# Performance work log

Hardware: AMD Instinct MI355X
Metric: run time of the kernel (lower is better)

## Reference

```python
import jax, jax.numpy as jnp
import numpy as np
import math

N_NODES = 50000
N_EDGES = 600000
EMBED_DIM = 128


def setup_inputs() -> dict:
    key = jax.random.key(0)
    k_emb, k_edge, k_w = jax.random.split(key, 3)
    emb = jax.random.normal(k_emb, (N_NODES, EMBED_DIM), dtype=jnp.float32) * 0.1
    edges = jax.random.randint(k_edge, (2, N_EDGES), 0, N_NODES, dtype=jnp.int64)
    std = 1.0 / math.sqrt(EMBED_DIM)
    # nn.Linear(2*embed_dim, embed_dim): weight [out, in]
    W = jax.random.uniform(k_w, (EMBED_DIM, 2 * EMBED_DIM), dtype=jnp.float32,
                           minval=-std, maxval=std)
    b = jnp.zeros((EMBED_DIM,), dtype=jnp.float32)
    gamma = jnp.ones((EMBED_DIM,), dtype=jnp.float32)
    beta = jnp.zeros((EMBED_DIM,), dtype=jnp.float32)
    return {"emb": emb, "edges": edges, "W": W, "b": b, "gamma": gamma, "beta": beta}


def reference(emb, edges, W, b, gamma, beta):
    bsz = emb.shape[0]
    row = edges[0]  # destination / output node per edge (spmm row index)
    col = edges[1]  # source node per edge (spmm col index)
    # edge attention logits: <emb[dst], emb[src]> per edge, then exp
    attn = jnp.exp(jnp.sum(emb[row] * emb[col], axis=-1))  # [E]
    # special_spmm with ones -> per-row sum of attention weights
    denom = jax.ops.segment_sum(attn, row, num_segments=bsz)  # [N]
    # special_spmm with emb -> exp-weighted scatter-add of source embeddings
    agg = jax.ops.segment_sum(attn[:, None] * emb[col], row, num_segments=bsz)  # [N, D]
    agg = agg / (denom[:, None] + 1e-20)
    # concat + linear
    x = jnp.concatenate([emb, agg], axis=-1) @ W.T + b  # [N, D]
    # layer norm (eps=1e-5, affine)
    mu = jnp.mean(x, axis=-1, keepdims=True)
    var = jnp.mean((x - mu) ** 2, axis=-1, keepdims=True)
    x = (x - mu) * jax.lax.rsqrt(var + 1e-5) * gamma + beta
    return x
```

## Files before the change

kernel.cpp:

```cpp
#include <hip/hip_runtime.h>
#include <math.h>

#define D 128
#define TWO_D 256
#define CAP 64
#define CCAP 3584
#define CHUNK 2048

typedef __bf16 v8bf __attribute__((ext_vector_type(8)));
typedef float  v4f  __attribute__((ext_vector_type(4)));
typedef unsigned short us4 __attribute__((ext_vector_type(4)));
typedef unsigned short v8us __attribute__((ext_vector_type(8)));

#define OFF_CNT      0u
#define OFF_COLBUF   200192u
#define OFF_CCNT     6600192u
#define OFF_COARSE   6601216u
#define OFF_WBF16    10271232u
#define OFF_EMBB     10336768u
#define WS_TIER_A    23136768u

__global__ __launch_bounds__(256) void k_cvt_bin(
    const float* __restrict__ emb, const float* __restrict__ W,
    const int* __restrict__ edges,
    __bf16* __restrict__ embb, __bf16* __restrict__ Wb,
    unsigned int* __restrict__ ccnt, unsigned int* __restrict__ coarse,
    int nEmb8, int nW8, int E, int binB, int NB)
{
    if ((int)blockIdx.x < binB) {
        __shared__ unsigned int hist[256];
        __shared__ unsigned int base[256];
        int tid = threadIdx.x;
        int e0  = blockIdx.x * CHUNK;
        hist[tid] = 0;
        __syncthreads();

        unsigned rs[CHUNK / 256];
        #pragma unroll
        for (int k = 0; k < CHUNK / 256; ++k) {
            int e = e0 + k * 256 + tid;
            if (e < E) {
                unsigned r  = (unsigned)edges[e];
                unsigned lp = atomicAdd(&hist[r >> 8], 1u);
                rs[k] = (r << 12) | lp;
            }
        }
        __syncthreads();
        if (tid < NB) {
            unsigned h = hist[tid];
            base[tid] = h ? atomicAdd(&ccnt[tid], h) : 0u;
        }
        __syncthreads();
        #pragma unroll
        for (int k = 0; k < CHUNK / 256; ++k) {
            int e = e0 + k * 256 + tid;
            if (e < E) {
                unsigned pk = rs[k];
                unsigned r  = pk >> 12;
                unsigned lp = pk & 0xFFFu;
                unsigned c  = (unsigned)edges[E + e];
                int bk = r >> 8;
                unsigned slot = base[bk] + lp;
                if (slot < CCAP)
                    coarse[(size_t)bk * CCAP + slot] = ((r & 255u) << 16) | c;
            }
        }
    } else {
        int tid = ((int)blockIdx.x - binB) * 256 + threadIdx.x;
        if (tid < nEmb8 + nW8) {
            const float* src;
            __bf16* dst;
            if (tid < nEmb8) { src = emb + (size_t)tid * 8; dst = embb + (size_t)tid * 8; }
            else { int j = (tid - nEmb8) * 8; src = W + j; dst = Wb + j; }
            float4 f0 = *(const float4*)(src);
            float4 f1 = *(const float4*)(src + 4);
            v8bf v;
            v[0] = (__bf16)f0.x; v[1] = (__bf16)f0.y; v[2] = (__bf16)f0.z; v[3] = (__bf16)f0.w;
            v[4] = (__bf16)f1.x; v[5] = (__bf16)f1.y; v[6] = (__bf16)f1.z; v[7] = (__bf16)f1.w;
            *(v8bf*)dst = v;
        }
    }
}

__global__ __launch_bounds__(256) void k_fine(
    const unsigned int* __restrict__ coarse,
    const unsigned int* __restrict__ ccnt,
    int* __restrict__ cnt, unsigned short* __restrict__ colbuf, int N)
{
    __shared__ __align__(16) unsigned short ftile[256 * CAP];
    __shared__ unsigned int fcnt[256];
    int tid = threadIdx.x;
    int b   = blockIdx.x;
    int r0  = b << 8;
    fcnt[tid] = 0;
    __syncthreads();

    unsigned mc = ccnt[b];
    if (mc > CCAP) mc = CCAP;
    for (unsigned i = tid; i < mc; i += 256) {
        unsigned p = coarse[(size_t)b * CCAP + i];
        unsigned rlo = p >> 16;
        unsigned c   = p & 0xFFFFu;
        unsigned lp  = atomicAdd(&fcnt[rlo], 1u);
        if (lp < CAP) ftile[rlo * CAP + lp] = (unsigned short)c;
    }
    __syncthreads();

    int r = r0 + tid;
    if (r < N) {
        unsigned d = fcnt[tid];
        cnt[r] = (int)(d > CAP ? CAP : d);
    }
    #pragma unroll
    for (int j = 0; j < 8; ++j) {
        int g  = j * 256 + tid;
        int rr = r0 + (g >> 3);
        if (rr < N)
            *(v8us*)(colbuf + (size_t)rr * CAP + (g & 7) * 8) =
                *(const v8us*)(ftile + (g >> 3) * CAP + (g & 7) * 8);
    }
}

__global__ __launch_bounds__(256) void gcn_agg_b(
    const __bf16* __restrict__ embb,
    const unsigned short* __restrict__ colbuf,
    const int* __restrict__ cnt,
    __bf16* __restrict__ aggb,
    int N)
{
    int wid  = threadIdx.x >> 6;
    int lane = threadIdx.x & 63;
    int il   = lane & 15;
    int slot = lane >> 4;
    int n    = blockIdx.x * 4 + wid;
    if (n >= N) return;

    v8bf a8 = *(const v8bf*)(embb + (size_t)n * D + il * 8);
    float af[8];
    #pragma unroll
    for (int q = 0; q < 8; ++q) af[q] = (float)a8[q];

    float acc[8];
    #pragma unroll
    for (int q = 0; q < 8; ++q) acc[q] = 0.f;
    float den = 0.f;

    int deg = cnt[n];
    if (deg > CAP) deg = CAP;
    const unsigned short* row = colbuf + (size_t)n * CAP;
    int nb = (deg + 7) >> 3;

    int i0 = 0, i1 = 0;
    if (slot < deg)     i0 = (int)row[slot];
    if (slot + 4 < deg) i1 = (int)row[slot + 4];
    v8bf r0 = *(const v8bf*)(embb + (size_t)i0 * D + il * 8);
    v8bf r1 = *(const v8bf*)(embb + (size_t)i1 * D + il * 8);

    for (int b = 0; b < nb; ++b) {
        int e   = b * 8;
        int rem = deg - e;
        bool v0 = (slot < rem);
        bool v1 = (slot + 4 < rem);

        int en   = e + 8;
        int remn = deg - en;
        bool hn  = (b + 1 < nb);
        int j0 = (hn && slot < remn)     ? (int)row[en + slot]     : 0;
        int j1 = (hn && slot + 4 < remn) ? (int)row[en + slot + 4] : 0;
        v8bf p0 = *(const v8bf*)(embb + (size_t)j0 * D + il * 8);
        v8bf p1 = *(const v8bf*)(embb + (size_t)j1 * D + il * 8);

        float f0[8], f1[8];
        #pragma unroll
        for (int q = 0; q < 8; ++q) { f0[q] = (float)r0[q]; f1[q] = (float)r1[q]; }
        float t0 = 0.f, t1 = 0.f;
        #pragma unroll
        for (int q = 0; q < 8; ++q) { t0 += af[q] * f0[q]; t1 += af[q] * f1[q]; }
        #pragma unroll
        for (int off = 1; off <= 8; off <<= 1) {
            t0 += __shfl_xor(t0, off, 16);
            t1 += __shfl_xor(t1, off, 16);
        }
        float w0 = v0 ? __expf(t0) : 0.f;
        float w1 = v1 ? __expf(t1) : 0.f;
        #pragma unroll
        for (int q = 0; q < 8; ++q) acc[q] += w0 * f0[q] + w1 * f1[q];
        den += w0 + w1;

        r0 = p0; r1 = p1;
    }

    #pragma unroll
    for (int q = 0; q < 8; ++q) {
        acc[q] += __shfl_xor(acc[q], 16, 64);
        acc[q] += __shfl_xor(acc[q], 32, 64);
    }
    den += __shfl_xor(den, 16, 64);
    den += __shfl_xor(den, 32, 64);

    if (slot == 0) {
        float inv = 1.0f / (den + 1e-20f);
        v8bf r;
        #pragma unroll
        for (int q = 0; q < 8; ++q) r[q] = (__bf16)(acc[q] * inv);
        *(v8bf*)(aggb + (size_t)n * 256 + il * 8) = r;
    }
}

__global__ __launch_bounds__(256) void gcn_node_b(
    const __bf16* __restrict__ embb,
    const __bf16* __restrict__ Wb,
    const float* __restrict__ bias,
    const float* __restrict__ gamma,
    const float* __restrict__ beta,
    float* __restrict__ out, int N)
{
    __shared__ __align__(16) __bf16 xt[64 * 256];

    int t    = threadIdx.x;
    int wave = t >> 6;
    int lane = t & 63;
    int n0   = blockIdx.x * 64;
    const __bf16* aggb = (const __bf16*)out;

    #pragma unroll
    for (int j = 0; j < 8; ++j) {
        int gf = j * 64 + lane;
        int ml = gf >> 5;
        int m  = wave * 16 + ml;
        int g  = gf & 31;
        int n  = n0 + m;
        v8bf v;
        if (n < N) {
            v = (g < 16) ? *(const v8bf*)(embb + (size_t)n * D + g * 8)
                         : *(const v8bf*)(aggb + (size_t)n * 256 + (g - 16) * 8);
        } else {
            #pragma unroll
            for (int q = 0; q < 8; ++q) v[q] = (__bf16)0.0f;
        }
        *(v8bf*)(xt + (m * 32 + (g ^ (m & 7))) * 8) = v;
    }

    int mrow = lane & 15;
    int quad = lane >> 4;
    int mloc = wave * 16 + mrow;

    v8bf a[8];
    #pragma unroll
    for (int kt = 0; kt < 8; ++kt) {
        int g = (kt * 4 + quad) ^ (mloc & 7);
        a[kt] = *(const v8bf*)(xt + (mloc * 32 + g) * 8);
    }

    float bi[8], gm[8], bt[8];
    #pragma unroll
    for (int ft = 0; ft < 8; ++ft) {
        int f = ft * 16 + mrow;
        bi[ft] = bias[f]; gm[ft] = gamma[f]; bt[ft] = beta[f];
    }

    v4f accf[8];
    #pragma unroll
    for (int ft = 0; ft < 8; ++ft)
        #pragma unroll
        for (int r = 0; r < 4; ++r) accf[ft][r] = 0.0f;

    #pragma unroll
    for (int kt = 0; kt < 8; ++kt) {
        #pragma unroll
        for (int ft = 0; ft < 8; ++ft) {
            v8bf b = *(const v8bf*)(Wb + (ft * 16 + mrow) * TWO_D + kt * 32 + quad * 8);
            accf[ft] = __builtin_amdgcn_mfma_f32_16x16x32_bf16(a[kt], b, accf[ft], 0, 0, 0);
        }
    }

    #pragma unroll
    for (int ft = 0; ft < 8; ++ft)
        #pragma unroll
        for (int r = 0; r < 4; ++r) accf[ft][r] += bi[ft];

    #pragma unroll
    for (int r = 0; r < 4; ++r) {
        float s = 0.f, s2 = 0.f;
        #pragma unroll
        for (int ft = 0; ft < 8; ++ft) {
            float x = accf[ft][r];
            s += x; s2 += x * x;
        }
        #pragma unroll
        for (int off = 1; off <= 8; off <<= 1) {
            s  += __shfl_xor(s,  off, 64);
            s2 += __shfl_xor(s2, off, 64);
        }
        float mu  = s * (1.0f / 128.0f);
        float var = s2 * (1.0f / 128.0f) - mu * mu;
        float ivn = rsqrtf(var + 1e-5f);
        int n = n0 + wave * 16 + quad * 4 + r;
        if (n < N) {
            #pragma unroll
            for (int ft = 0; ft < 8; ++ft) {
                int f = ft * 16 + mrow;
                out[(size_t)n * D + f] = (accf[ft][r] - mu) * ivn * gm[ft] + bt[ft];
            }
        }
    }
}

__global__ __launch_bounds__(256) void gcn_edge_attn(
    const float* __restrict__ emb, const int* __restrict__ edges,
    float* __restrict__ agg, float* __restrict__ denom, int E) {
    int e    = (int)((blockIdx.x * 256u + threadIdx.x) >> 6);
    int lane = threadIdx.x & 63;
    if (e >= E) return;
    int row = edges[e];
    int col = edges[E + e];
    const float2 a = *(const float2*)(emb + (size_t)row * D + lane * 2);
    const float2 c = *(const float2*)(emb + (size_t)col * D + lane * 2);
    float s = a.x * c.x + a.y * c.y;
    #pragma unroll
    for (int off = 32; off >= 1; off >>= 1) s += __shfl_xor(s, off, 64);
    float attn = expf(s);
    float* dst = agg + (size_t)row * D + lane * 2;
    unsafeAtomicAdd(dst,     attn * c.x);
    unsafeAtomicAdd(dst + 1, attn * c.y);
    if (lane == 0) unsafeAtomicAdd(denom + row, attn);
}

__global__ __launch_bounds__(256) void gcn_node_fallback(
    const float* __restrict__ emb, const float* __restrict__ W,
    const float* __restrict__ bias, const float* __restrict__ gamma,
    const float* __restrict__ beta, const float* __restrict__ denom,
    float* __restrict__ out, int N) {
    __shared__ float scat[2][TWO_D];
    __shared__ float sred[2][4];
    int tid  = threadIdx.x;
    int g    = tid >> 7;
    int o    = tid & 127;
    int lane = tid & 63;
    int wig  = (tid >> 6) & 1;
    for (int n0 = blockIdx.x * 2; n0 < N; n0 += gridDim.x * 2) {
        int n = n0 + g;
        bool act = (n < N);
        if (act) {
            float ev  = emb[(size_t)n * D + o];
            float inv = 1.0f / (denom[n] + 1e-20f);
            scat[g][o]     = ev;
            scat[g][D + o] = out[(size_t)n * D + o] * inv;
        }
        __syncthreads();
        float acc = 0.f;
        if (act) {
            const float4* wr = (const float4*)(W + (size_t)o * TWO_D);
            #pragma unroll 4
            for (int k4 = 0; k4 < TWO_D / 4; ++k4) {
                float4 w = wr[k4];
                float4 a = *(const float4*)(&scat[g][k4 * 4]);
                acc += w.x * a.x + w.y * a.y + w.z * a.z + w.w * a.w;
            }
            acc += bias[o];
        }
        float s = acc, s2 = acc * acc;
        #pragma unroll
        for (int off = 32; off >= 1; off >>= 1) {
            s  += __shfl_xor(s,  off, 64);
            s2 += __shfl_xor(s2, off, 64);
        }
        if (lane == 0) { sred[g][wig * 2] = s; sred[g][wig * 2 + 1] = s2; }
        __syncthreads();
        if (act) {
            float ts  = sred[g][0] + sred[g][2];
            float ts2 = sred[g][1] + sred[g][3];
            float mu  = ts * (1.0f / 128.0f);
            float var = ts2 * (1.0f / 128.0f) - mu * mu;
            float inv = rsqrtf(var + 1e-5f);
            out[(size_t)n * D + o] = (acc - mu) * inv * gamma[o] + beta[o];
        }
        __syncthreads();
    }
}

extern "C" void kernel_launch(void* const* d_in, const int* in_sizes, int n_in,
                              void* d_out, int out_size, void* d_ws, size_t ws_size,
                              hipStream_t stream) {
    const float* emb   = (const float*)d_in[0];
    const int*   edges = (const int*)  d_in[1];
    const float* W     = (const float*)d_in[2];
    const float* bias  = (const float*)d_in[3];
    const float* gamma = (const float*)d_in[4];
    const float* beta  = (const float*)d_in[5];
    float* out = (float*)d_out;

    int N = in_sizes[0] / D;
    int E = in_sizes[1] / 2;

    if (ws_size >= (size_t)WS_TIER_A) {
        char* ws = (char*)d_ws;
        int*            cnt    = (int*)            (ws + OFF_CNT);
        unsigned short* colbuf = (unsigned short*) (ws + OFF_COLBUF);
        unsigned int*   ccnt   = (unsigned int*)   (ws + OFF_CCNT);
        unsigned int*   coarse = (unsigned int*)   (ws + OFF_COARSE);
        __bf16*         Wb     = (__bf16*)         (ws + OFF_WBF16);
        __bf16*         embb   = (__bf16*)         (ws + OFF_EMBB);

        int nEmb8 = N * D / 8;
        int nW8   = D * TWO_D / 8;
        int cvtB  = (nEmb8 + nW8 + 255) / 256;
        int binB  = (E + CHUNK - 1) / CHUNK;
        int NB    = (N + 255) >> 8;

        hipMemsetAsync(ccnt, 0, 1024, stream);
        k_cvt_bin<<<binB + cvtB, 256, 0, stream>>>(
            emb, W, edges, embb, Wb, ccnt, coarse, nEmb8, nW8, E, binB, NB);
        k_fine   <<<NB, 256, 0, stream>>>(coarse, ccnt, cnt, colbuf, N);
        gcn_agg_b<<<(N + 3) / 4, 256, 0, stream>>>(embb, colbuf, cnt,
                                                   (__bf16*)out, N);
        gcn_node_b<<<(N + 63) / 64, 256, 0, stream>>>(embb, Wb, bias, gamma,
                                                      beta, out, N);
    } else {
        float* denom = (float*)d_ws;
        hipMemsetAsync(out,   0, (size_t)N * D * sizeof(float), stream);
        hipMemsetAsync(denom, 0, (size_t)N * sizeof(float), stream);
        gcn_edge_attn<<<(E + 3) / 4, 256, 0, stream>>>(emb, edges, out, denom, E);
        gcn_node_fallback<<<512, 256, 0, stream>>>(emb, W, bias, gamma, beta,
                                                   denom, out, N);
    }
}
```

Measured before the change: 171.8 us.

## Fuse attention aggregation into node linear+layernorm kernel via shared memory

Merges the per-node attention aggregation kernel into the GEMM+LayerNorm kernel. Each wave aggregates 16 nodes in turn and writes the bf16 results straight into the shared-memory tile instead of round-tripping them through global memory. This removes one launch and the aggregate write and re-read. In exchange, parallelism drops from one wave per node to one wave per 16 nodes processed serially, and the software prefetch of the next neighbour batch is gone, so gather latency is exposed more.

```diff
diff --git a/kernel.cpp b/kernel.cpp
--- a/kernel.cpp
+++ b/kernel.cpp
@@ -9,7 +9,6 @@
 
 typedef __bf16 v8bf __attribute__((ext_vector_type(8)));
 typedef float  v4f  __attribute__((ext_vector_type(4)));
-typedef unsigned short us4 __attribute__((ext_vector_type(4)));
 typedef unsigned short v8us __attribute__((ext_vector_type(8)));
 
 #define OFF_CNT      0u
@@ -121,94 +120,10 @@
     }
 }
 
-__global__ __launch_bounds__(256) void gcn_agg_b(
+__global__ __launch_bounds__(256) void gcn_fused(
     const __bf16* __restrict__ embb,
     const unsigned short* __restrict__ colbuf,
     const int* __restrict__ cnt,
-    __bf16* __restrict__ aggb,
-    int N)
-{
-    int wid  = threadIdx.x >> 6;
-    int lane = threadIdx.x & 63;
-    int il   = lane & 15;
-    int slot = lane >> 4;
-    int n    = blockIdx.x * 4 + wid;
-    if (n >= N) return;
-
-    v8bf a8 = *(const v8bf*)(embb + (size_t)n * D + il * 8);
-    float af[8];
-    #pragma unroll
-    for (int q = 0; q < 8; ++q) af[q] = (float)a8[q];
-
-    float acc[8];
-    #pragma unroll
-    for (int q = 0; q < 8; ++q) acc[q] = 0.f;
-    float den = 0.f;
-
-    int deg = cnt[n];
-    if (deg > CAP) deg = CAP;
-    const unsigned short* row = colbuf + (size_t)n * CAP;
-    int nb = (deg + 7) >> 3;
-
-    int i0 = 0, i1 = 0;
-    if (slot < deg)     i0 = (int)row[slot];
-    if (slot + 4 < deg) i1 = (int)row[slot + 4];
-    v8bf r0 = *(const v8bf*)(embb + (size_t)i0 * D + il * 8);
-    v8bf r1 = *(const v8bf*)(embb + (size_t)i1 * D + il * 8);
-
-    for (int b = 0; b < nb; ++b) {
-        int e   = b * 8;
-        int rem = deg - e;
-        bool v0 = (slot < rem);
-        bool v1 = (slot + 4 < rem);
-
-        int en   = e + 8;
-        int remn = deg - en;
-        bool hn  = (b + 1 < nb);
-        int j0 = (hn && slot < remn)     ? (int)row[en + slot]     : 0;
-        int j1 = (hn && slot + 4 < remn) ? (int)row[en + slot + 4] : 0;
-        v8bf p0 = *(const v8bf*)(embb + (size_t)j0 * D + il * 8);
-        v8bf p1 = *(const v8bf*)(embb + (size_t)j1 * D + il * 8);
-
-        float f0[8], f1[8];
-        #pragma unroll
-        for (int q = 0; q < 8; ++q) { f0[q] = (float)r0[q]; f1[q] = (float)r1[q]; }
-        float t0 = 0.f, t1 = 0.f;
-        #pragma unroll
-        for (int q = 0; q < 8; ++q) { t0 += af[q] * f0[q]; t1 += af[q] * f1[q]; }
-        #pragma unroll
-        for (int off = 1; off <= 8; off <<= 1) {
-            t0 += __shfl_xor(t0, off, 16);
-            t1 += __shfl_xor(t1, off, 16);
-        }
-        float w0 = v0 ? __expf(t0) : 0.f;
-        float w1 = v1 ? __expf(t1) : 0.f;
-        #pragma unroll
-        for (int q = 0; q < 8; ++q) acc[q] += w0 * f0[q] + w1 * f1[q];
-        den += w0 + w1;
-
-        r0 = p0; r1 = p1;
-    }
-
-    #pragma unroll
-    for (int q = 0; q < 8; ++q) {
-        acc[q] += __shfl_xor(acc[q], 16, 64);
-        acc[q] += __shfl_xor(acc[q], 32, 64);
-    }
-    den += __shfl_xor(den, 16, 64);
-    den += __shfl_xor(den, 32, 64);
-
-    if (slot == 0) {
-        float inv = 1.0f / (den + 1e-20f);
-        v8bf r;
-        #pragma unroll
-        for (int q = 0; q < 8; ++q) r[q] = (__bf16)(acc[q] * inv);
-        *(v8bf*)(aggb + (size_t)n * 256 + il * 8) = r;
-    }
-}
-
-__global__ __launch_bounds__(256) void gcn_node_b(
-    const __bf16* __restrict__ embb,
     const __bf16* __restrict__ Wb,
     const float* __restrict__ bias,
     const float* __restrict__ gamma,
@@ -220,25 +135,96 @@
     int t    = threadIdx.x;
     int wave = t >> 6;
     int lane = t & 63;
+    int il   = lane & 15;
+    int slot = lane >> 4;
     int n0   = blockIdx.x * 64;
-    const __bf16* aggb = (const __bf16*)out;
-
-    #pragma unroll
-    for (int j = 0; j < 8; ++j) {
+
+    #pragma unroll
+    for (int j = 0; j < 4; ++j) {
         int gf = j * 64 + lane;
-        int ml = gf >> 5;
+        int ml = gf >> 4;
+        int g  = gf & 15;
         int m  = wave * 16 + ml;
-        int g  = gf & 31;
         int n  = n0 + m;
         v8bf v;
         if (n < N) {
-            v = (g < 16) ? *(const v8bf*)(embb + (size_t)n * D + g * 8)
-                         : *(const v8bf*)(aggb + (size_t)n * 256 + (g - 16) * 8);
+            v = *(const v8bf*)(embb + (size_t)n * D + g * 8);
         } else {
             #pragma unroll
             for (int q = 0; q < 8; ++q) v[q] = (__bf16)0.0f;
         }
         *(v8bf*)(xt + (m * 32 + (g ^ (m & 7))) * 8) = v;
+    }
+
+    for (int ml = 0; ml < 16; ++ml) {
+        int m = wave * 16 + ml;
+        int n = n0 + m;
+        if (n < N) {
+            v8bf a8 = *(const v8bf*)(xt + (m * 32 + (il ^ (m & 7))) * 8);
+            float af[8];
+            #pragma unroll
+            for (int q = 0; q < 8; ++q) af[q] = (float)a8[q];
+
+            float acc[8];
+            #pragma unroll
+            for (int q = 0; q < 8; ++q) acc[q] = 0.f;
+            float den = 0.f;
+
+            int deg = cnt[n];
+            if (deg > CAP) deg = CAP;
+            const unsigned short* row = colbuf + (size_t)n * CAP;
+            int nb = (deg + 7) >> 3;
+
+            for (int b = 0; b < nb; ++b) {
+                int e   = b * 8;
+                int rem = deg - e;
+                bool v0 = (slot < rem);
+                bool v1 = (slot + 4 < rem);
+                int i0 = v0 ? (int)row[e + slot]     : 0;
+                int i1 = v1 ? (int)row[e + slot + 4] : 0;
+                v8bf r0 = *(const v8bf*)(embb + (size_t)i0 * D + il * 8);
+                v8bf r1 = *(const v8bf*)(embb + (size_t)i1 * D + il * 8);
+                float f0[8], f1[8];
+                #pragma unroll
+                for (int q = 0; q < 8; ++q) { f0[q] = (float)r0[q]; f1[q] = (float)r1[q]; }
+                float t0 = 0.f, t1 = 0.f;
+                #pragma unroll
+                for (int q = 0; q < 8; ++q) { t0 += af[q] * f0[q]; t1 += af[q] * f1[q]; }
+                #pragma unroll
+                for (int off = 1; off <= 8; off <<= 1) {
+                    t0 += __shfl_xor(t0, off, 16);
+                    t1 += __shfl_xor(t1, off, 16);
+                }
+                float w0 = v0 ? __expf(t0) : 0.f;
+                float w1 = v1 ? __expf(t1) : 0.f;
+                #pragma unroll
+                for (int q = 0; q < 8; ++q) acc[q] += w0 * f0[q] + w1 * f1[q];
+                den += w0 + w1;
+            }
+
+            #pragma unroll
+            for (int q = 0; q < 8; ++q) {
+                acc[q] += __shfl_xor(acc[q], 16, 64);
+                acc[q] += __shfl_xor(acc[q], 32, 64);
+            }
+            den += __shfl_xor(den, 16, 64);
+            den += __shfl_xor(den, 32, 64);
+
+            if (slot == 0) {
+                float inv = 1.0f / (den + 1e-20f);
+                v8bf r;
+                #pragma unroll
+                for (int q = 0; q < 8; ++q) r[q] = (__bf16)(acc[q] * inv);
+                *(v8bf*)(xt + (m * 32 + ((16 + il) ^ (m & 7))) * 8) = r;
+            }
+        } else {
+            if (slot == 0) {
+                v8bf z;
+                #pragma unroll
+                for (int q = 0; q < 8; ++q) z[q] = (__bf16)0.0f;
+                *(v8bf*)(xt + (m * 32 + ((16 + il) ^ (m & 7))) * 8) = z;
+            }
+        }
     }
 
     int mrow = lane & 15;
@@ -412,10 +398,8 @@
         k_cvt_bin<<<binB + cvtB, 256, 0, stream>>>(
             emb, W, edges, embb, Wb, ccnt, coarse, nEmb8, nW8, E, binB, NB);
         k_fine   <<<NB, 256, 0, stream>>>(coarse, ccnt, cnt, colbuf, N);
-        gcn_agg_b<<<(N + 3) / 4, 256, 0, stream>>>(embb, colbuf, cnt,
-                                                   (__bf16*)out, N);
-        gcn_node_b<<<(N + 63) / 64, 256, 0, stream>>>(embb, Wb, bias, gamma,
-                                                      beta, out, N);
+        gcn_fused<<<(N + 63) / 64, 256, 0, stream>>>(embb, colbuf, cnt, Wb,
+                                                     bias, gamma, beta, out, N);
     } else {
         float* denom = (float*)d_ws;
         hipMemsetAsync(out,   0, (size_t)N * D * sizeof(float), stream);
```

After: 184.5 us. 7.4% more time.
